# Kernel optimization log

Measured on AMD Instinct MI355X. Metric: run time of the kernel, lower is better.

The kernel has to match this reference:

```python
import jax, jax.numpy as jnp
import numpy as np

EPS = 1e-6
NUM_HEADS = 16

def _rmsnorm(h, w):
    hf = h.astype(jnp.float32)
    var = jnp.mean(hf * hf, axis=-1, keepdims=True)
    return (w * (hf * jax.lax.rsqrt(var + EPS))).astype(h.dtype)

def _rotary(t, cos, sin):
    # t: [B,N,H,hd]; cos/sin: [N, hd//2]
    tf = t.astype(jnp.float32)
    tr = tf[..., 0::2]
    ti = tf[..., 1::2]
    c = cos[None, :, None, :]
    s = sin[None, :, None, :]
    out_r = tr * c - ti * s
    out_i = tr * s + ti * c
    out = jnp.stack([out_r, out_i], axis=-1).reshape(t.shape)
    return out.astype(t.dtype)

def setup_inputs() -> dict:
    key = jax.random.key(0)
    ks = jax.random.split(key, 8)
    B, N, C = 2, 2048, 1024
    hd = C // NUM_HEADS
    x = jax.random.normal(ks[0], (B, N, C), jnp.float32)
    qkv_w = jax.random.normal(ks[1], (3 * C, C), jnp.float32) * (C ** -0.5)
    q_norm_w = jnp.ones((hd,), jnp.float32)
    k_norm_w = jnp.ones((hd,), jnp.float32)
    proj_w = jax.random.normal(ks[2], (C, C), jnp.float32) * (C ** -0.5)
    proj_b = jnp.zeros((C,), jnp.float32)
    # rotary freqs_cis = exp(i * theta): unit-magnitude cos/sin
    inv_freq = 1.0 / (10000.0 ** (jnp.arange(0, hd, 2, dtype=jnp.float32) / hd))
    ang = jnp.arange(N, dtype=jnp.float32)[:, None] * inv_freq[None, :]
    pos_cos = jnp.cos(ang)
    pos_sin = jnp.sin(ang)
    mask = jnp.tril(jnp.ones((N, N), dtype=bool))
    return {"x": x, "qkv_w": qkv_w, "q_norm_w": q_norm_w, "k_norm_w": k_norm_w,
            "proj_w": proj_w, "proj_b": proj_b, "pos_cos": pos_cos,
            "pos_sin": pos_sin, "mask": mask}

def reference(x, qkv_w, q_norm_w, k_norm_w, proj_w, proj_b, pos_cos, pos_sin, mask):
    B, N, C = x.shape
    H = NUM_HEADS
    hd = C // H
    qkv = (x @ qkv_w.T).reshape(B, N, 3, H, hd)
    q, k, v = qkv[:, :, 0], qkv[:, :, 1], qkv[:, :, 2]  # [B,N,H,hd]
    q = _rmsnorm(q, q_norm_w)
    k = _rmsnorm(k, k_norm_w)
    q = _rotary(q, pos_cos, pos_sin)
    k = _rotary(k, pos_cos, pos_sin)
    q = q.transpose(0, 2, 1, 3)  # [B,H,N,hd]
    k = k.transpose(0, 2, 1, 3)
    v = v.transpose(0, 2, 1, 3)
    scale = hd ** -0.5
    scores = jnp.einsum('bhqd,bhkd->bhqk', q, k) * scale
    scores = jnp.where(mask[None, None, :, :], scores, jnp.float32(-1e30))
    attn = jax.nn.softmax(scores, axis=-1)
    out = jnp.einsum('bhqk,bhkd->bhqd', attn, v)
    out = out.transpose(0, 2, 1, 3).reshape(B, N, C)
    return out @ proj_w.T + proj_b
```

## Files before the change

kernel.cpp:

```cpp
#include <hip/hip_runtime.h>

using u16 = unsigned short;
using short4v = __attribute__((ext_vector_type(4))) short;
using short8 = __attribute__((ext_vector_type(8))) short;
using floatx4 = __attribute__((ext_vector_type(4))) float;

__device__ __forceinline__ float bf2f(u16 h) {
  union { unsigned int u; float f; } v;
  v.u = ((unsigned int)h) << 16;
  return v.f;
}
__device__ __forceinline__ u16 f2bf(float f) {
  union { float f; unsigned int u; } v;
  v.f = f;
  unsigned int u = v.u;
  return (u16)((u + 0x7FFFu + ((u >> 16) & 1u)) >> 16);
}
__device__ __forceinline__ u16 f2bf_rtz(float f) {
  union { float f; unsigned int u; } v;
  v.f = f;
  return (u16)(v.u >> 16);
}

typedef const __attribute__((address_space(1))) unsigned int* gas_t;
typedef __attribute__((address_space(3))) unsigned int* las_t;
__device__ __forceinline__ void gl_lds16(const u16* g, u16* l) {
  __builtin_amdgcn_global_load_lds((gas_t)(const void*)g, (las_t)(void*)l, 16,
                                   0, 0);
}

#define QSCALE 0.180336880111f

__global__ __launch_bounds__(256) void cvt_all(
    const float* __restrict__ x, const float* __restrict__ wq,
    const float* __restrict__ wp, u16* __restrict__ xb, u16* __restrict__ wqb,
    u16* __restrict__ wpb) {
  int i = blockIdx.x * 256 + threadIdx.x;
  const float* src;
  u16* dst;
  int off;
  if (i < 1048576) {
    src = x; dst = xb; off = i;
  } else if (i < 1048576 + 786432) {
    src = wq; dst = wqb; off = i - 1048576;
  } else {
    src = wp; dst = wpb; off = i - 1835008;
  }
  float4 v = ((const float4*)src)[off];
  ushort4 o;
  o.x = f2bf(v.x);
  o.y = f2bf(v.y);
  o.z = f2bf(v.z);
  o.w = f2bf(v.w);
  ((ushort4*)dst)[off] = o;
}

template <int BIAS, int OUTBF16, int MT>
__global__ __launch_bounds__(256) void gemm_nt(
    const u16* __restrict__ A, const u16* __restrict__ B,
    const float* __restrict__ bias, void* __restrict__ Cout,
    int M, int N, int K) {
  constexpr int ROWS_A = MT * 32;
  __shared__ u16 As[ROWS_A * 32];
  __shared__ u16 Bs[128 * 32];
  const int tid = threadIdx.x;
  const int lane = tid & 63;
  const int wave = tid >> 6;
  const int col = lane & 15;
  const int quad = lane >> 4;
  const int bm = blockIdx.y * ROWS_A;
  const int bn = blockIdx.x * 128;
  const int wm = (wave >> 1) * (MT * 16);
  const int wn = (wave & 1) * 64;

  floatx4 acc[MT][4] = {};

  for (int kb = 0; kb < K; kb += 32) {
    __syncthreads();
#pragma unroll
    for (int c = tid; c < ROWS_A * 4; c += 256)
      gl_lds16(A + (size_t)(bm + (c >> 2)) * K + kb + (c & 3) * 8, As + c * 8);
#pragma unroll
    for (int c = tid; c < 512; c += 256)
      gl_lds16(B + (size_t)(bn + (c >> 2)) * K + kb + (c & 3) * 8, Bs + c * 8);
    __syncthreads();

    short8 af[MT], bfr[4];
#pragma unroll
    for (int i = 0; i < MT; i++)
      af[i] = *(const short8*)(As + (wm + i * 16 + col) * 32 + quad * 8);
#pragma unroll
    for (int i = 0; i < 4; i++)
      bfr[i] = *(const short8*)(Bs + (wn + i * 16 + col) * 32 + quad * 8);
#pragma unroll
    for (int mi = 0; mi < MT; mi++)
#pragma unroll
      for (int ni = 0; ni < 4; ni++)
        acc[mi][ni] = __builtin_amdgcn_mfma_f32_16x16x32_bf16(
            af[mi], bfr[ni], acc[mi][ni], 0, 0, 0);
  }

#pragma unroll
  for (int mi = 0; mi < MT; mi++) {
#pragma unroll
    for (int ni = 0; ni < 4; ni++) {
#pragma unroll
      for (int r = 0; r < 4; r++) {
        int row = bm + wm + mi * 16 + quad * 4 + r;
        int c = bn + wn + ni * 16 + col;
        float v = acc[mi][ni][r];
        if (BIAS) v += bias[c];
        if (OUTBF16)
          ((u16*)Cout)[(size_t)row * N + c] = f2bf(v);
        else
          ((float*)Cout)[(size_t)row * N + c] = v;
      }
    }
  }
}

__global__ __launch_bounds__(256) void rope_v(
    const u16* __restrict__ qkv, const float* __restrict__ qw,
    const float* __restrict__ kw, const float* __restrict__ pcos,
    const float* __restrict__ psin, u16* __restrict__ Qb,
    u16* __restrict__ Kb, u16* __restrict__ Vt) {
  __shared__ u16 T[64 * 68];
  const int bh = blockIdx.x;
  const int n0 = blockIdx.y * 64;
  const int b = bh >> 4, h = bh & 15;
  const int tid = threadIdx.x;
  const int lane = tid & 63;
  const int wave = tid >> 6;

  const float qwl = qw[lane];
  const float kwl = kw[lane];
  for (int tt = 0; tt < 16; tt++) {
    const int n = n0 + wave * 16 + tt;
    const int t = b * 2048 + n;
    const u16* base = qkv + (size_t)t * 3072 + h * 64 + lane;
    float qv = bf2f(base[0]);
    float kv = bf2f(base[1024]);

    float sq = qv * qv, sk = kv * kv;
#pragma unroll
    for (int off = 32; off; off >>= 1) {
      sq += __shfl_xor(sq, off);
      sk += __shfl_xor(sk, off);
    }
    float qn = qv * rsqrtf(sq * (1.0f / 64.0f) + 1e-6f) * qwl;
    float kn = kv * rsqrtf(sk * (1.0f / 64.0f) + 1e-6f) * kwl;

    const int i = lane >> 1;
    const float c = pcos[n * 32 + i];
    const float s = psin[n * 32 + i];
    float qp = __shfl_xor(qn, 1);
    float kp = __shfl_xor(kn, 1);
    float qr, kr;
    if (lane & 1) {
      qr = qp * s + qn * c;
      kr = kp * s + kn * c;
    } else {
      qr = qn * c - qp * s;
      kr = kn * c - kp * s;
    }
    qr *= QSCALE;

    const size_t o = ((size_t)bh * 2048 + n) * 64 + lane;
    Qb[o] = f2bf(qr);
    Kb[o] = f2bf(kr);
  }

  const int q = tid & 7;
  const int r = tid >> 3;
#pragma unroll
  for (int rr = r; rr < 64; rr += 32) {
    short8 v = *(const short8*)(qkv + (size_t)(b * 2048 + n0 + rr) * 3072 +
                                2048 + h * 64 + q * 8);
    *(short8*)&T[rr * 68 + q * 8] = v;
  }
  __syncthreads();
#pragma unroll
  for (int dd = r; dd < 64; dd += 32) {
    short8 o;
#pragma unroll
    for (int j = 0; j < 8; j++) o[j] = T[(q * 8 + j) * 68 + dd];
    *(short8*)(Vt + (size_t)(bh * 64 + dd) * 2048 + n0 + q * 8) = o;
  }
}

#define PSTR 68
__global__ __launch_bounds__(256) void attn_flash(
    const u16* __restrict__ Q, const u16* __restrict__ Kk,
    const u16* __restrict__ Vt, u16* __restrict__ O) {
  __shared__ u16 Ks[2][2][64 * 32];
  __shared__ u16 Vs[2][2][64 * 32];
  __shared__ u16 Pb[4][16 * PSTR];
  const int id = blockIdx.x;
  const int bh = id & 31;
  const int pair = id >> 5;
  const int tileA = 31 - pair;
  const int tileB = pair;
  const int tid = threadIdx.x;
  const int lane = tid & 63;
  const int wave = tid >> 6;
  const int col = lane & 15;
  const int quad = lane >> 4;
  const int srow = tid >> 2;
  const int sswz = ((tid & 3) ^ (srow & 3)) * 8;
  const int rq = (quad ^ (col & 3)) * 8;

  const u16* Qh = Q + (size_t)bh * 2048 * 64;
  const u16* Kh = Kk + (size_t)bh * 2048 * 64;
  const u16* Vh = Vt + (size_t)bh * 64 * 2048;
  const int b = bh >> 4, h = bh & 15;

  const int q0A = tileA * 64 + wave * 16;
  const int q0B = tileB * 64 + wave * 16;
  const int nsA = tileA + 1;
  const int nsB = tileB + 1;

  short8 aqA[2], aqB[2];
#pragma unroll
  for (int ks = 0; ks < 2; ks++) {
    aqA[ks] =
        *(const short8*)(Qh + (size_t)(q0A + col) * 64 + ks * 32 + quad * 8);
    aqB[ks] =
        *(const short8*)(Qh + (size_t)(q0B + col) * 64 + ks * 32 + quad * 8);
  }

  short8 ones;
#pragma unroll
  for (int j = 0; j < 8; j++) ones[j] = (short)0x3F80;

  floatx4 accO[4] = {};
  floatx4 lacc = {};
  int cur = 0;

  auto step = [&](int j0, int jnext, int q0, const short8* aq) {
    if (jnext >= 0) {
#pragma unroll
      for (int half = 0; half < 2; half++) {
        gl_lds16(Kh + (size_t)(jnext + srow) * 64 + half * 32 + sswz,
                 &Ks[cur ^ 1][half][0] + tid * 8);
        gl_lds16(Vh + (size_t)srow * 2048 + jnext + half * 32 + sswz,
                 &Vs[cur ^ 1][half][0] + tid * 8);
      }
    }

    floatx4 s[4] = {};
#pragma unroll
    for (int nt = 0; nt < 4; nt++) {
#pragma unroll
      for (int ks = 0; ks < 2; ks++) {
        short8 bk = *(const short8*)&Ks[cur][ks][(nt * 16 + col) * 32 + rq];
        s[nt] =
            __builtin_amdgcn_mfma_f32_16x16x32_bf16(bk, aq[ks], s[nt], 0, 0, 0);
      }
    }

    if (j0 + 63 <= q0) {
#pragma unroll
      for (int nt = 0; nt < 4; nt++) {
        short4v pk;
#pragma unroll
        for (int r = 0; r < 4; r++)
          pk[r] = (short)f2bf_rtz(exp2f(s[nt][r]));
        *(short4v*)&Pb[wave][col * PSTR + nt * 16 + quad * 4] = pk;
      }
    } else {
      const int qg = q0 + col;
#pragma unroll
      for (int nt = 0; nt < 4; nt++) {
        const int jgb = j0 + nt * 16 + quad * 4;
        short4v pk;
#pragma unroll
        for (int r = 0; r < 4; r++) {
          float pv = (jgb + r <= qg) ? exp2f(s[nt][r]) : 0.0f;
          pk[r] = (short)f2bf_rtz(pv);
        }
        *(short4v*)&Pb[wave][col * PSTR + nt * 16 + quad * 4] = pk;
      }
    }

    short8 ap[2];
#pragma unroll
    for (int kf = 0; kf < 2; kf++)
      ap[kf] = *(const short8*)&Pb[wave][col * PSTR + kf * 32 + quad * 8];

#pragma unroll
    for (int kf = 0; kf < 2; kf++)
      lacc = __builtin_amdgcn_mfma_f32_16x16x32_bf16(ap[kf], ones, lacc, 0, 0,
                                                     0);

#pragma unroll
    for (int nt = 0; nt < 4; nt++) {
#pragma unroll
      for (int kf = 0; kf < 2; kf++) {
        short8 bv = *(const short8*)&Vs[cur][kf][(nt * 16 + col) * 32 + rq];
        accO[nt] = __builtin_amdgcn_mfma_f32_16x16x32_bf16(ap[kf], bv,
                                                           accO[nt], 0, 0, 0);
      }
    }

    __syncthreads();
    cur ^= 1;
  };

  auto finish = [&](int q0) {
    float lrec[4];
#pragma unroll
    for (int r = 0; r < 4; r++) lrec[r] = 1.0f / lacc[r];
#pragma unroll
    for (int nt = 0; nt < 4; nt++) {
#pragma unroll
      for (int r = 0; r < 4; r++) {
        int qg = q0 - wave * 16 + wave * 16 + quad * 4 + r;
        int d = nt * 16 + col;
        O[((size_t)(b * 2048 + (q0 + quad * 4 + r)) * 16 + h) * 64 + d] =
            f2bf(accO[nt][r] * lrec[r]);
        (void)qg;
      }
    }
#pragma unroll
    for (int nt = 0; nt < 4; nt++) accO[nt] = (floatx4){0.f, 0.f, 0.f, 0.f};
    lacc = (floatx4){0.f, 0.f, 0.f, 0.f};
  };

#pragma unroll
  for (int half = 0; half < 2; half++) {
    gl_lds16(Kh + (size_t)srow * 64 + half * 32 + sswz,
             &Ks[0][half][0] + tid * 8);
    gl_lds16(Vh + (size_t)srow * 2048 + half * 32 + sswz,
             &Vs[0][half][0] + tid * 8);
  }
  __syncthreads();

  for (int kt = 0; kt < nsA; kt++)
    step(kt * 64, (kt + 1 < nsA) ? (kt + 1) * 64 : 0, q0A, aqA);
  finish(q0A);

  for (int kt = 0; kt < nsB; kt++)
    step(kt * 64, (kt + 1 < nsB) ? (kt + 1) * 64 : -1, q0B, aqB);
  finish(q0B);
}

extern "C" void kernel_launch(void* const* d_in, const int* in_sizes, int n_in,
                              void* d_out, int out_size, void* d_ws,
                              size_t ws_size, hipStream_t stream) {
  const float* x = (const float*)d_in[0];
  const float* qkv_w = (const float*)d_in[1];
  const float* q_norm_w = (const float*)d_in[2];
  const float* k_norm_w = (const float*)d_in[3];
  const float* proj_w = (const float*)d_in[4];
  const float* proj_b = (const float*)d_in[5];
  const float* pos_cos = (const float*)d_in[6];
  const float* pos_sin = (const float*)d_in[7];

  char* ws = (char*)d_ws;
  u16* xb = (u16*)ws;
  u16* wqkvb = (u16*)(ws + 8388608);
  u16* wprojb = (u16*)(ws + 14680064);
  u16* qkv = (u16*)(ws + 16777216);
  u16* Qb = (u16*)(ws + 41943040);
  u16* Kb = (u16*)(ws + 50331648);
  u16* Vt = (u16*)(ws + 58720256);
  u16* AO = (u16*)(ws + 67108864);

  cvt_all<<<8192, 256, 0, stream>>>(x, qkv_w, proj_w, xb, wqkvb, wprojb);

  gemm_nt<0, 1, 4><<<dim3(24, 32), 256, 0, stream>>>(xb, wqkvb, nullptr, qkv,
                                                     4096, 3072, 1024);

  rope_v<<<dim3(32, 32), 256, 0, stream>>>(qkv, q_norm_w, k_norm_w, pos_cos,
                                           pos_sin, Qb, Kb, Vt);

  attn_flash<<<dim3(512), 256, 0, stream>>>(Qb, Kb, Vt, AO);

  gemm_nt<1, 0, 2><<<dim3(8, 64), 256, 0, stream>>>(AO, wprojb, proj_b,
                                                    (float*)d_out, 4096, 1024,
                                                    1024);
}
```

Before: 211.4 us.

## Split attention keys across waves, keep P in registers, reduce partial outputs in LDS

The flash attention kernel now gives each wave a 16-key slice of every 64-key tile for all 64 queries, where before each wave owned 16 queries across all keys. The score output layout then feeds directly into 16x16x16 MFMAs for P·V and the row sums, so the LDS round-trip for P is gone. At the end of each query tile, the partial O accumulators and row sums from the four waves are reduced through LDS (reusing the K/V buffers). The cost is four times the accumulator registers, a multi-barrier cross-wave reduction per tile, and the loss of the XOR swizzle on K/V shared-memory loads.

After: 261.7 us. 1.24x slower.

```diff
diff --git a/kernel.cpp b/kernel.cpp
--- a/kernel.cpp
+++ b/kernel.cpp
@@ -27,6 +27,17 @@
 __device__ __forceinline__ void gl_lds16(const u16* g, u16* l) {
   __builtin_amdgcn_global_load_lds((gas_t)(const void*)g, (las_t)(void*)l, 16,
                                    0, 0);
+}
+
+#define MFMA32 __builtin_amdgcn_mfma_f32_16x16x32_bf16
+__device__ __forceinline__ floatx4 mfma16(short4v a, short4v b, floatx4 c) {
+#if __has_builtin(__builtin_amdgcn_mfma_f32_16x16x16bf16_1k)
+  return __builtin_amdgcn_mfma_f32_16x16x16bf16_1k(a, b, c, 0, 0, 0);
+#else
+  short8 a8 = {a[0], a[1], a[2], a[3], 0, 0, 0, 0};
+  short8 b8 = {b[0], b[1], b[2], b[3], 0, 0, 0, 0};
+  return MFMA32(a8, b8, c, 0, 0, 0);
+#endif
 }
 
 #define QSCALE 0.180336880111f
@@ -96,8 +107,7 @@
     for (int mi = 0; mi < MT; mi++)
 #pragma unroll
       for (int ni = 0; ni < 4; ni++)
-        acc[mi][ni] = __builtin_amdgcn_mfma_f32_16x16x32_bf16(
-            af[mi], bfr[ni], acc[mi][ni], 0, 0, 0);
+        acc[mi][ni] = MFMA32(af[mi], bfr[ni], acc[mi][ni], 0, 0, 0);
   }
 
 #pragma unroll
@@ -188,13 +198,12 @@
   }
 }
 
-#define PSTR 68
 __global__ __launch_bounds__(256) void attn_flash(
     const u16* __restrict__ Q, const u16* __restrict__ Kk,
     const u16* __restrict__ Vt, u16* __restrict__ O) {
   __shared__ u16 Ks[2][2][64 * 32];
   __shared__ u16 Vs[2][2][64 * 32];
-  __shared__ u16 Pb[4][16 * PSTR];
+  __shared__ float lsc[4][64];
   const int id = blockIdx.x;
   const int bh = id & 31;
   const int pair = id >> 5;
@@ -206,141 +215,185 @@
   const int col = lane & 15;
   const int quad = lane >> 4;
   const int srow = tid >> 2;
-  const int sswz = ((tid & 3) ^ (srow & 3)) * 8;
-  const int rq = (quad ^ (col & 3)) * 8;
+  const int spc = (tid & 3) * 8;
 
   const u16* Qh = Q + (size_t)bh * 2048 * 64;
   const u16* Kh = Kk + (size_t)bh * 2048 * 64;
   const u16* Vh = Vt + (size_t)bh * 64 * 2048;
   const int b = bh >> 4, h = bh & 15;
 
-  const int q0A = tileA * 64 + wave * 16;
-  const int q0B = tileB * 64 + wave * 16;
+  const int q0A = tileA * 64;
+  const int q0B = tileB * 64;
   const int nsA = tileA + 1;
   const int nsB = tileB + 1;
 
-  short8 aqA[2], aqB[2];
-#pragma unroll
-  for (int ks = 0; ks < 2; ks++) {
-    aqA[ks] =
-        *(const short8*)(Qh + (size_t)(q0A + col) * 64 + ks * 32 + quad * 8);
-    aqB[ks] =
-        *(const short8*)(Qh + (size_t)(q0B + col) * 64 + ks * 32 + quad * 8);
-  }
-
-  short8 ones;
-#pragma unroll
-  for (int j = 0; j < 8; j++) ones[j] = (short)0x3F80;
-
-  floatx4 accO[4] = {};
-  floatx4 lacc = {};
+  short4v ones4;
+#pragma unroll
+  for (int j = 0; j < 4; j++) ones4[j] = (short)0x3F80;
+
+  floatx4 accO[4][4] = {};
+  floatx4 lacc[4] = {};
+  short8 aq[4][2];
   int cur = 0;
 
-  auto step = [&](int j0, int jnext, int q0, const short8* aq) {
+  auto load_aq = [&](int q0) {
+#pragma unroll
+    for (int qg = 0; qg < 4; qg++)
+#pragma unroll
+      for (int ks = 0; ks < 2; ks++)
+        aq[qg][ks] = *(const short8*)(Qh + (size_t)(q0 + qg * 16 + col) * 64 +
+                                      ks * 32 + quad * 8);
+  };
+
+  auto step = [&](int j0, int jnext, int q0) {
     if (jnext >= 0) {
 #pragma unroll
       for (int half = 0; half < 2; half++) {
-        gl_lds16(Kh + (size_t)(jnext + srow) * 64 + half * 32 + sswz,
+        gl_lds16(Kh + (size_t)(jnext + srow) * 64 + half * 32 + spc,
                  &Ks[cur ^ 1][half][0] + tid * 8);
-        gl_lds16(Vh + (size_t)srow * 2048 + jnext + half * 32 + sswz,
+        gl_lds16(Vh + (size_t)srow * 2048 + jnext + half * 32 + spc,
                  &Vs[cur ^ 1][half][0] + tid * 8);
       }
     }
 
+    short8 ak[2];
+#pragma unroll
+    for (int ks = 0; ks < 2; ks++)
+      ak[ks] = *(const short8*)&Ks[cur][ks][(wave * 16 + col) * 32 + quad * 8];
+    short4v bv[4];
+#pragma unroll
+    for (int dg = 0; dg < 4; dg++)
+      bv[dg] = *(const short4v*)&Vs[cur][wave >> 1]
+                   [(dg * 16 + col) * 32 + (wave & 1) * 16 + quad * 4];
+
     floatx4 s[4] = {};
 #pragma unroll
-    for (int nt = 0; nt < 4; nt++) {
-#pragma unroll
-      for (int ks = 0; ks < 2; ks++) {
-        short8 bk = *(const short8*)&Ks[cur][ks][(nt * 16 + col) * 32 + rq];
-        s[nt] =
-            __builtin_amdgcn_mfma_f32_16x16x32_bf16(bk, aq[ks], s[nt], 0, 0, 0);
-      }
-    }
-
+    for (int qg = 0; qg < 4; qg++)
+#pragma unroll
+      for (int ks = 0; ks < 2; ks++)
+        s[qg] = MFMA32(ak[ks], aq[qg][ks], s[qg], 0, 0, 0);
+
+    short4v pa[4];
     if (j0 + 63 <= q0) {
 #pragma unroll
-      for (int nt = 0; nt < 4; nt++) {
-        short4v pk;
+      for (int qg = 0; qg < 4; qg++)
 #pragma unroll
         for (int r = 0; r < 4; r++)
-          pk[r] = (short)f2bf_rtz(exp2f(s[nt][r]));
-        *(short4v*)&Pb[wave][col * PSTR + nt * 16 + quad * 4] = pk;
-      }
+          pa[qg][r] = (short)f2bf_rtz(exp2f(s[qg][r]));
     } else {
-      const int qg = q0 + col;
-#pragma unroll
-      for (int nt = 0; nt < 4; nt++) {
-        const int jgb = j0 + nt * 16 + quad * 4;
-        short4v pk;
+      const int keyg = j0 + wave * 16 + quad * 4;
+#pragma unroll
+      for (int qg = 0; qg < 4; qg++) {
+        const int qq = q0 + qg * 16 + col;
 #pragma unroll
         for (int r = 0; r < 4; r++) {
-          float pv = (jgb + r <= qg) ? exp2f(s[nt][r]) : 0.0f;
-          pk[r] = (short)f2bf_rtz(pv);
+          float pv = (keyg + r <= qq) ? exp2f(s[qg][r]) : 0.0f;
+          pa[qg][r] = (short)f2bf_rtz(pv);
         }
-        *(short4v*)&Pb[wave][col * PSTR + nt * 16 + quad * 4] = pk;
-      }
-    }
-
-    short8 ap[2];
-#pragma unroll
-    for (int kf = 0; kf < 2; kf++)
-      ap[kf] = *(const short8*)&Pb[wave][col * PSTR + kf * 32 + quad * 8];
-
-#pragma unroll
-    for (int kf = 0; kf < 2; kf++)
-      lacc = __builtin_amdgcn_mfma_f32_16x16x32_bf16(ap[kf], ones, lacc, 0, 0,
-                                                     0);
-
-#pragma unroll
-    for (int nt = 0; nt < 4; nt++) {
-#pragma unroll
-      for (int kf = 0; kf < 2; kf++) {
-        short8 bv = *(const short8*)&Vs[cur][kf][(nt * 16 + col) * 32 + rq];
-        accO[nt] = __builtin_amdgcn_mfma_f32_16x16x32_bf16(ap[kf], bv,
-                                                           accO[nt], 0, 0, 0);
-      }
-    }
+      }
+    }
+
+#pragma unroll
+    for (int qg = 0; qg < 4; qg++)
+      lacc[qg] = mfma16(pa[qg], ones4, lacc[qg]);
+
+#pragma unroll
+    for (int dg = 0; dg < 4; dg++)
+#pragma unroll
+      for (int qg = 0; qg < 4; qg++)
+        accO[qg][dg] = mfma16(pa[qg], bv[dg], accO[qg][dg]);
 
     __syncthreads();
     cur ^= 1;
   };
 
   auto finish = [&](int q0) {
-    float lrec[4];
-#pragma unroll
-    for (int r = 0; r < 4; r++) lrec[r] = 1.0f / lacc[r];
-#pragma unroll
-    for (int nt = 0; nt < 4; nt++) {
-#pragma unroll
-      for (int r = 0; r < 4; r++) {
-        int qg = q0 - wave * 16 + wave * 16 + quad * 4 + r;
-        int d = nt * 16 + col;
-        O[((size_t)(b * 2048 + (q0 + quad * 4 + r)) * 16 + h) * 64 + d] =
-            f2bf(accO[nt][r] * lrec[r]);
-        (void)qg;
-      }
-    }
-#pragma unroll
-    for (int nt = 0; nt < 4; nt++) accO[nt] = (floatx4){0.f, 0.f, 0.f, 0.f};
-    lacc = (floatx4){0.f, 0.f, 0.f, 0.f};
+    const int sbuf = cur ^ 1;
+    float* const sc0 = (float*)&Ks[sbuf][0][0];
+    float* const sc1 = (float*)&Ks[sbuf][1][0];
+    float* const sc2 = (float*)&Vs[sbuf][0][0];
+    float* const sc3 = (float*)&Vs[sbuf][1][0];
+
+    {
+      floatx4 lv = lacc[0];
+      lv = ((col & 3) == 1) ? lacc[1] : lv;
+      lv = ((col & 3) == 2) ? lacc[2] : lv;
+      lv = ((col & 3) == 3) ? lacc[3] : lv;
+      *(floatx4*)&lsc[wave][(col & 3) * 16 + quad * 4] = lv;
+    }
+
+#pragma unroll
+    for (int r = 1; r < 4; r++) {
+#pragma unroll
+      for (int w2 = 0; w2 < 4; w2++) {
+        if (wave == w2) {
+          const int dst = (w2 + r) & 3;
+          float* d = dst == 0 ? sc0 : dst == 1 ? sc1 : dst == 2 ? sc2 : sc3;
+#pragma unroll
+          for (int qg = 0; qg < 4; qg++)
+            *(floatx4*)&d[col * 64 + (((qg * 4 + quad) ^ col) & 15) * 4] =
+                accO[qg][dst];
+        }
+      }
+      __syncthreads();
+#pragma unroll
+      for (int w2 = 0; w2 < 4; w2++) {
+        if (wave == w2) {
+          const float* m = w2 == 0 ? sc0 : w2 == 1 ? sc1 : w2 == 2 ? sc2 : sc3;
+#pragma unroll
+          for (int qg = 0; qg < 4; qg++)
+            accO[qg][w2] +=
+                *(const floatx4*)&m[col * 64 +
+                                    (((qg * 4 + quad) ^ col) & 15) * 4];
+        }
+      }
+      __syncthreads();
+    }
+
+#pragma unroll
+    for (int qg = 0; qg < 4; qg++) {
+      floatx4 lt = *(const floatx4*)&lsc[0][qg * 16 + quad * 4];
+#pragma unroll
+      for (int w2 = 1; w2 < 4; w2++)
+        lt += *(const floatx4*)&lsc[w2][qg * 16 + quad * 4];
+#pragma unroll
+      for (int w2 = 0; w2 < 4; w2++) {
+        if (wave == w2) {
+#pragma unroll
+          for (int r = 0; r < 4; r++) {
+            const int qq = q0 + qg * 16 + quad * 4 + r;
+            O[((size_t)(b * 2048 + qq) * 16 + h) * 64 + w2 * 16 + col] =
+                f2bf(accO[qg][w2][r] / lt[r]);
+          }
+        }
+      }
+    }
+#pragma unroll
+    for (int qg = 0; qg < 4; qg++) {
+#pragma unroll
+      for (int dg = 0; dg < 4; dg++)
+        accO[qg][dg] = (floatx4){0.f, 0.f, 0.f, 0.f};
+      lacc[qg] = (floatx4){0.f, 0.f, 0.f, 0.f};
+    }
   };
 
+  load_aq(q0A);
 #pragma unroll
   for (int half = 0; half < 2; half++) {
-    gl_lds16(Kh + (size_t)srow * 64 + half * 32 + sswz,
+    gl_lds16(Kh + (size_t)srow * 64 + half * 32 + spc,
              &Ks[0][half][0] + tid * 8);
-    gl_lds16(Vh + (size_t)srow * 2048 + half * 32 + sswz,
+    gl_lds16(Vh + (size_t)srow * 2048 + half * 32 + spc,
              &Vs[0][half][0] + tid * 8);
   }
   __syncthreads();
 
   for (int kt = 0; kt < nsA; kt++)
-    step(kt * 64, (kt + 1 < nsA) ? (kt + 1) * 64 : 0, q0A, aqA);
+    step(kt * 64, (kt + 1 < nsA) ? (kt + 1) * 64 : 0, q0A);
   finish(q0A);
 
+  load_aq(q0B);
   for (int kt = 0; kt < nsB; kt++)
-    step(kt * 64, (kt + 1 < nsB) ? (kt + 1) * 64 : -1, q0B, aqB);
+    step(kt * 64, (kt + 1 < nsB) ? (kt + 1) * 64 : -1, q0B);
   finish(q0B);
 }
 
```
